# Kernel optimization log

Measured on AMD Instinct MI355X. Metric: run time of the kernel, lower is better.

## Reference

```python
import jax, jax.numpy as jnp
import numpy as np

OUT_F, IN_F = 16384, 4096
TOKENS = 8192
PALETTE = 256


def setup_inputs() -> dict:
    key = jax.random.key(0)
    k1, k2, k3, k4 = jax.random.split(key, 4)
    input = jax.random.normal(k1, (TOKENS, IN_F), dtype=jnp.float32)
    weight_idx = jax.random.randint(k2, (OUT_F, IN_F), 0, PALETTE, dtype=jnp.int32)
    lookup_table = jax.random.normal(k3, (PALETTE,), dtype=jnp.float32)
    bias = jax.random.normal(k4, (OUT_F,), dtype=jnp.float32)
    return {"input": input, "weight_idx": weight_idx, "lookup_table": lookup_table, "bias": bias}


def reference(input, weight_idx, lookup_table, bias):
    # Dequantize: LUT gather expands uint8 indices to full-precision weights [out, in]
    full_weights = lookup_table[weight_idx]
    # F.linear: y = x @ W^T + b
    return jnp.einsum('ti,oi->to', input, full_weights) + bias
```

## Files before the change

### kernel.cpp

```cpp
#include <hip/hip_runtime.h>
#include <stdint.h>

#define TOKENS 8192
#define OUT_F  16384
#define IN_F   4096

typedef short bf16x8 __attribute__((ext_vector_type(8)));
typedef float f32x4  __attribute__((ext_vector_type(4)));

__device__ __forceinline__ unsigned short bf16_rne(float f) {
    union { float f; unsigned int u; } v; v.f = f;
    unsigned int u = v.u;
    u += 0x7fffu + ((u >> 16) & 1u);
    return (unsigned short)(u >> 16);
}

__device__ __forceinline__ unsigned int pack_bf16x2(float a, float b) {
    return (unsigned int)bf16_rne(a) | ((unsigned int)bf16_rne(b) << 16);
}

__device__ __forceinline__ void async_cp16(const void* gptr, void* ldsptr) {
    __builtin_amdgcn_global_load_lds(
        (const __attribute__((address_space(1))) unsigned int*)gptr,
        (__attribute__((address_space(3))) unsigned int*)ldsptr,
        16, 0, 0);
}

__global__ __launch_bounds__(256) void cvt_input_kernel(
    const float* __restrict__ in, unsigned short* __restrict__ out, int n8)
{
    int i = blockIdx.x * 256 + threadIdx.x;
    if (i >= n8) return;
    size_t base = (size_t)i * 8;
    float4 a = *(const float4*)(in + base);
    float4 b = *(const float4*)(in + base + 4);
    uint4 p;
    p.x = pack_bf16x2(a.x, a.y);  p.y = pack_bf16x2(a.z, a.w);
    p.z = pack_bf16x2(b.x, b.y);  p.w = pack_bf16x2(b.z, b.w);
    *(uint4*)(out + base) = p;
}

__global__ __launch_bounds__(256) void dequant_kernel(
    const int* __restrict__ idx, const float* __restrict__ lut,
    unsigned short* __restrict__ out, int n8)
{
    __shared__ float slut[256];
    slut[threadIdx.x] = lut[threadIdx.x];
    __syncthreads();
    int i = blockIdx.x * 256 + threadIdx.x;
    if (i >= n8) return;
    size_t base = (size_t)i * 8;
    int4 i0 = *(const int4*)(idx + base);
    int4 i1 = *(const int4*)(idx + base + 4);
    uint4 p;
    p.x = pack_bf16x2(slut[i0.x], slut[i0.y]);
    p.y = pack_bf16x2(slut[i0.z], slut[i0.w]);
    p.z = pack_bf16x2(slut[i1.x], slut[i1.y]);
    p.w = pack_bf16x2(slut[i1.z], slut[i1.w]);
    *(uint4*)(out + base) = p;
}

__global__ __launch_bounds__(512, 2) void palett_gemm256(
    const unsigned short* __restrict__ A,
    const unsigned short* __restrict__ B,
    const float* __restrict__ bias,
    float* __restrict__ out)
{
    __shared__ __align__(16) char sm[131072];

    const int t    = threadIdx.x;
    const int w    = t >> 6;
    const int l    = t & 63;
    const int quad = l >> 4;
    const int r16  = l & 15;
    const int wr   = w >> 2;
    const int wc   = w & 3;

    const int orig = blockIdx.y * gridDim.x + blockIdx.x;
    const int swzb = (orig & 7) * 256 + (orig >> 3);
    const int n0   = (swzb & 63) << 8;
    const int m0   = (swzb >> 6) << 8;

    const int srow = w * 16 + (l >> 3);
    const int scol = ((l & 7) ^ (l >> 3)) << 3;
    const unsigned short* pA = A + (size_t)(m0 + srow) * IN_F + scol;
    const unsigned short* pB = B + (size_t)(n0 + srow) * IN_F + scol;

    const int cswz  = (r16 & 7) << 4;
    const int col0  = (quad * 16) ^ cswz;
    const int col1  = (64 + quad * 16) ^ cswz;
    const int arow  = r16 * 128;
    const int abase = wr * 16384;
    const int bbase = 32768 + (wc >> 1) * 16384 + (wc & 1) * 8192;

    f32x4  acc[8][4] = {};
    bf16x8 rA[4][2], rB0[2][2], rB1[2][2];

#define BARRIER() asm volatile("s_barrier" ::: "memory")

#define STAGE(P, HOFF, LOFF, KOFF) do {                                          \
    async_cp16((P) + (size_t)(HOFF) * IN_F + (KOFF), sm + (LOFF) + w * 2048);    \
    async_cp16((P) + (size_t)((HOFF) + 8) * IN_F + (KOFF),                       \
               sm + (LOFF) + w * 2048 + 1024);                                   \
} while (0)

#define READ_A(RB_, MH) do {                                                     \
    _Pragma("unroll")                                                            \
    for (int i_ = 0; i_ < 4; ++i_) {                                             \
        rA[i_][0] = *(const bf16x8*)(sm + (RB_) + abase + ((MH)*4 + i_)*2048 + arow + col0); \
        rA[i_][1] = *(const bf16x8*)(sm + (RB_) + abase + ((MH)*4 + i_)*2048 + arow + col1); \
    }                                                                            \
} while (0)

#define READ_B(DST, RB_, NH) do {                                                \
    _Pragma("unroll")                                                            \
    for (int j_ = 0; j_ < 2; ++j_) {                                             \
        DST[j_][0] = *(const bf16x8*)(sm + (RB_) + bbase + ((NH)*2 + j_)*2048 + arow + col0); \
        DST[j_][1] = *(const bf16x8*)(sm + (RB_) + bbase + ((NH)*2 + j_)*2048 + arow + col1); \
    }                                                                            \
} while (0)

#define MFMA_Q(MH, NH, RB) do {                                                  \
    _Pragma("unroll")                                                            \
    for (int i_ = 0; i_ < 4; ++i_) {                                             \
        _Pragma("unroll")                                                        \
        for (int j_ = 0; j_ < 2; ++j_) {                                         \
            acc[(MH)*4+i_][(NH)*2+j_] = __builtin_amdgcn_mfma_f32_16x16x32_bf16( \
                rA[i_][0], RB[j_][0], acc[(MH)*4+i_][(NH)*2+j_], 0, 0, 0);       \
            acc[(MH)*4+i_][(NH)*2+j_] = __builtin_amdgcn_mfma_f32_16x16x32_bf16( \
                rA[i_][1], RB[j_][1], acc[(MH)*4+i_][(NH)*2+j_], 0, 0, 0);       \
        }                                                                        \
    }                                                                            \
} while (0)

#define TILE(RB_, WB_, KB_, KA_) do {                                            \
                                        \
    STAGE(pB, 0,   (WB_) + 32768, KB_);                                          \
    STAGE(pB, 128, (WB_) + 49152, KB_);                                          \
    READ_A(RB_, 0);                                                              \
    READ_B(rB0, RB_, 0);                                                         \
    __builtin_amdgcn_s_setprio(1);                                               \
    MFMA_Q(0, 0, rB0);                                                           \
    __builtin_amdgcn_s_setprio(0);                                               \
    BARRIER();                                                                   \
        \
    READ_B(rB1, RB_, 1);                                                         \
    __builtin_amdgcn_s_setprio(1);                                               \
    MFMA_Q(0, 1, rB1);                                                           \
    __builtin_amdgcn_s_setprio(0);                                               \
    READ_A(RB_, 1);                                                              \
    asm volatile("s_waitcnt lgkmcnt(0)" ::: "memory");                           \
    BARRIER();           \
                                             \
    STAGE(pA, 0,   (RB_) + 0,     KA_);                                          \
    STAGE(pA, 128, (RB_) + 16384, KA_);                                          \
    __builtin_amdgcn_s_setprio(1);                                               \
    MFMA_Q(1, 0, rB0);                                                           \
    __builtin_amdgcn_s_setprio(0);                                               \
    BARRIER();                                                                   \
             \
    __builtin_amdgcn_s_setprio(1);                                               \
    MFMA_Q(1, 1, rB1);                                                           \
    __builtin_amdgcn_s_setprio(0);                                               \
    asm volatile("s_waitcnt vmcnt(4)" ::: "memory");                             \
    BARRIER();                                                                   \
} while (0)

    STAGE(pA, 0,   0,             0);
    STAGE(pA, 128, 16384,         0);
    STAGE(pB, 0,   32768,         0);
    STAGE(pB, 128, 49152,         0);
    STAGE(pA, 0,   65536 + 0,     64);
    STAGE(pA, 128, 65536 + 16384, 64);
    asm volatile("s_waitcnt vmcnt(4)" ::: "memory");
    BARRIER();

#pragma unroll 1
    for (int it = 0; it < 32; ++it) {
        const int tt = 2 * it;
        const int kB0 = ((tt + 1) & 63) * 64;
        const int kA0 = ((tt + 2) & 63) * 64;
        const int kB1 = ((tt + 2) & 63) * 64;
        const int kA1 = ((tt + 3) & 63) * 64;
        TILE(0,     65536, kB0, kA0);
        TILE(65536, 0,     kB1, kA1);
    }
    asm volatile("s_waitcnt vmcnt(0)" ::: "memory");

#undef TILE
#undef MFMA_Q
#undef READ_B
#undef READ_A
#undef STAGE
#undef BARRIER

    float bj[4];
#pragma unroll
    for (int j = 0; j < 4; ++j) bj[j] = bias[n0 + wc * 64 + j * 16 + r16];

#pragma unroll
    for (int mf = 0; mf < 8; ++mf) {
        const int mrow = m0 + wr * 128 + mf * 16 + quad * 4;
#pragma unroll
        for (int nf = 0; nf < 4; ++nf) {
            const int n = n0 + wc * 64 + nf * 16 + r16;
#pragma unroll
            for (int v = 0; v < 4; ++v)
                out[(size_t)(mrow + v) * OUT_F + n] = acc[mf][nf][v] + bj[nf];
        }
    }
}

__global__ __launch_bounds__(256) void palett_gemm_fused(
    const float* __restrict__ Af,
    const int* __restrict__ Widx,
    const float* __restrict__ lut,
    const float* __restrict__ bias,
    float* __restrict__ out)
{
    __shared__ __align__(16) unsigned short smA[128 * 32];
    __shared__ __align__(16) unsigned short smB[128 * 32];
    __shared__ float slut[256];

    const int t    = threadIdx.x;
    const int w    = t >> 6;
    const int l    = t & 63;
    const int quad = l >> 4;
    const int r16  = l & 15;
    const int wr   = w >> 1;
    const int wc   = w & 1;

    const int m0 = blockIdx.y * 128;
    const int n0 = blockIdx.x * 128;

    const int g0  = t * 8;
    const int row = g0 >> 5;
    const int col = g0 & 31;

    char* const smA_c = (char*)smA;
    char* const smB_c = (char*)smB;

    slut[t] = lut[t];
    __syncthreads();

    uint32_t aoff[4], boff[4];
#pragma unroll
    for (int i = 0; i < 4; ++i) {
        aoff[i] = (uint32_t)(((wr * 64 + i * 16 + r16) * 32 + quad * 8) * 2);
        boff[i] = (uint32_t)(((wc * 64 + i * 16 + r16) * 32 + quad * 8) * 2);
    }

    f32x4 acc[4][4] = {};

    const float* af0 = Af + (size_t)(m0 + row) * IN_F + col;
    const float* af1 = Af + (size_t)(m0 + row + 64) * IN_F + col;
    const int*   wi0 = Widx + (size_t)(n0 + row) * IN_F + col;
    const int*   wi1 = Widx + (size_t)(n0 + row + 64) * IN_F + col;

    for (int k0 = 0; k0 < IN_F; k0 += 32) {
        float4 x0 = *(const float4*)(af0 + k0);
        float4 x1 = *(const float4*)(af0 + k0 + 4);
        uint4 p;
        p.x = pack_bf16x2(x0.x, x0.y); p.y = pack_bf16x2(x0.z, x0.w);
        p.z = pack_bf16x2(x1.x, x1.y); p.w = pack_bf16x2(x1.z, x1.w);
        *(uint4*)(smA_c + t * 16) = p;
        x0 = *(const float4*)(af1 + k0);
        x1 = *(const float4*)(af1 + k0 + 4);
        p.x = pack_bf16x2(x0.x, x0.y); p.y = pack_bf16x2(x0.z, x0.w);
        p.z = pack_bf16x2(x1.x, x1.y); p.w = pack_bf16x2(x1.z, x1.w);
        *(uint4*)(smA_c + 4096 + t * 16) = p;

        int4 j0 = *(const int4*)(wi0 + k0);
        int4 j1 = *(const int4*)(wi0 + k0 + 4);
        p.x = pack_bf16x2(slut[j0.x], slut[j0.y]);
        p.y = pack_bf16x2(slut[j0.z], slut[j0.w]);
        p.z = pack_bf16x2(slut[j1.x], slut[j1.y]);
        p.w = pack_bf16x2(slut[j1.z], slut[j1.w]);
        *(uint4*)(smB_c + t * 16) = p;
        j0 = *(const int4*)(wi1 + k0);
        j1 = *(const int4*)(wi1 + k0 + 4);
        p.x = pack_bf16x2(slut[j0.x], slut[j0.y]);
        p.y = pack_bf16x2(slut[j0.z], slut[j0.w]);
        p.z = pack_bf16x2(slut[j1.x], slut[j1.y]);
        p.w = pack_bf16x2(slut[j1.z], slut[j1.w]);
        *(uint4*)(smB_c + 4096 + t * 16) = p;
        __syncthreads();

        bf16x8 afr[4], bfr[4];
#pragma unroll
        for (int i = 0; i < 4; ++i) afr[i] = *(const bf16x8*)(smA_c + aoff[i]);
#pragma unroll
        for (int j = 0; j < 4; ++j) bfr[j] = *(const bf16x8*)(smB_c + boff[j]);
#pragma unroll
        for (int i = 0; i < 4; ++i)
#pragma unroll
            for (int j = 0; j < 4; ++j)
                acc[i][j] = __builtin_amdgcn_mfma_f32_16x16x32_bf16(
                    afr[i], bfr[j], acc[i][j], 0, 0, 0);
        __syncthreads();
    }

    float bj[4];
#pragma unroll
    for (int j = 0; j < 4; ++j) bj[j] = bias[n0 + wc * 64 + j * 16 + r16];

#pragma unroll
    for (int i = 0; i < 4; ++i) {
        const int mbase = m0 + wr * 64 + i * 16 + quad * 4;
#pragma unroll
        for (int j = 0; j < 4; ++j) {
            const int n = n0 + wc * 64 + j * 16 + r16;
#pragma unroll
            for (int v = 0; v < 4; ++v) {
                out[(size_t)(mbase + v) * OUT_F + n] = acc[i][j][v] + bj[j];
            }
        }
    }
}

extern "C" void kernel_launch(void* const* d_in, const int* in_sizes, int n_in,
                              void* d_out, int out_size, void* d_ws, size_t ws_size,
                              hipStream_t stream) {
    const float* input = (const float*)d_in[0];
    const int*   widx  = (const int*)d_in[1];
    const float* lut   = (const float*)d_in[2];
    const float* bias  = (const float*)d_in[3];
    float* out = (float*)d_out;

    const size_t aBytes = (size_t)TOKENS * IN_F * sizeof(unsigned short);
    const size_t bBytes = (size_t)OUT_F  * IN_F * sizeof(unsigned short);

    if (ws_size >= aBytes + bBytes) {
        unsigned short* wsA = (unsigned short*)d_ws;
        unsigned short* wsB = (unsigned short*)((char*)d_ws + aBytes);
        const int nA8 = (TOKENS * IN_F) / 8;
        const int nB8 = (OUT_F  * IN_F) / 8;
        cvt_input_kernel<<<(nA8 + 255) / 256, 256, 0, stream>>>(input, wsA, nA8);
        dequant_kernel<<<(nB8 + 255) / 256, 256, 0, stream>>>(widx, lut, wsB, nB8);
        dim3 grid2(OUT_F / 256, TOKENS / 256);
        palett_gemm256<<<grid2, 512, 0, stream>>>(wsA, wsB, bias, out);
    } else {
        dim3 grid(OUT_F / 128, TOKENS / 128);
        palett_gemm_fused<<<grid, 256, 0, stream>>>(input, widx, lut, bias, out);
    }
}
```

Before: 1.580 ms.

## Switch GEMM main loop to 32x32x16 bf16 MFMA with k-step pipelined LDS reads

```diff
diff --git a/kernel.cpp b/kernel.cpp
--- a/kernel.cpp
+++ b/kernel.cpp
@@ -5,8 +5,9 @@
 #define OUT_F  16384
 #define IN_F   4096
 
-typedef short bf16x8 __attribute__((ext_vector_type(8)));
-typedef float f32x4  __attribute__((ext_vector_type(4)));
+typedef short bf16x8  __attribute__((ext_vector_type(8)));
+typedef float f32x4   __attribute__((ext_vector_type(4)));
+typedef float f32x16  __attribute__((ext_vector_type(16)));
 
 __device__ __forceinline__ unsigned short bf16_rne(float f) {
     union { float f; unsigned int u; } v; v.f = f;
@@ -71,8 +72,8 @@
     const int t    = threadIdx.x;
     const int w    = t >> 6;
     const int l    = t & 63;
-    const int quad = l >> 4;
-    const int r16  = l & 15;
+    const int l31  = l & 31;
+    const int hi   = l >> 5;
     const int wr   = w >> 2;
     const int wc   = w & 3;
 
@@ -86,17 +87,13 @@
     const unsigned short* pA = A + (size_t)(m0 + srow) * IN_F + scol;
     const unsigned short* pB = B + (size_t)(n0 + srow) * IN_F + scol;
 
-    const int cswz  = (r16 & 7) << 4;
-    const int col0  = (quad * 16) ^ cswz;
-    const int col1  = (64 + quad * 16) ^ cswz;
-    const int arow  = r16 * 128;
+    const int arow  = l31 * 128;
+    const int bcol  = ((hi ^ (l & 7)) << 4);
     const int abase = wr * 16384;
     const int bbase = 32768 + (wc >> 1) * 16384 + (wc & 1) * 8192;
 
-    f32x4  acc[8][4] = {};
-    bf16x8 rA[4][2], rB0[2][2], rB1[2][2];
-
-#define BARRIER() asm volatile("s_barrier" ::: "memory")
+    f32x16 acc[4][2] = {};
+    bf16x8 fA[2][4], fB[2][2];
 
 #define STAGE(P, HOFF, LOFF, KOFF) do {                                          \
     async_cp16((P) + (size_t)(HOFF) * IN_F + (KOFF), sm + (LOFF) + w * 2048);    \
@@ -104,66 +101,46 @@
                sm + (LOFF) + w * 2048 + 1024);                                   \
 } while (0)
 
-#define READ_A(RB_, MH) do {                                                     \
+#define READ_K(S_, RB_, KK_) do {                                                \
     _Pragma("unroll")                                                            \
-    for (int i_ = 0; i_ < 4; ++i_) {                                             \
-        rA[i_][0] = *(const bf16x8*)(sm + (RB_) + abase + ((MH)*4 + i_)*2048 + arow + col0); \
-        rA[i_][1] = *(const bf16x8*)(sm + (RB_) + abase + ((MH)*4 + i_)*2048 + arow + col1); \
+    for (int m_ = 0; m_ < 4; ++m_)                                               \
+        fA[S_][m_] = *(const bf16x8*)(sm + (RB_) + abase + m_ * 4096 + arow      \
+                                      + (((KK_) * 32) ^ bcol));                  \
+    _Pragma("unroll")                                                            \
+    for (int n_ = 0; n_ < 2; ++n_)                                               \
+        fB[S_][n_] = *(const bf16x8*)(sm + (RB_) + bbase + n_ * 4096 + arow      \
+                                      + (((KK_) * 32) ^ bcol));                  \
+} while (0)
+
+#define MFMA_K(S_) do {                                                          \
+    __builtin_amdgcn_s_setprio(1);                                               \
+    _Pragma("unroll")                                                            \
+    for (int m_ = 0; m_ < 4; ++m_) {                                             \
+        _Pragma("unroll")                                                        \
+        for (int n_ = 0; n_ < 2; ++n_)                                           \
+            acc[m_][n_] = __builtin_amdgcn_mfma_f32_32x32x16_bf16(               \
+                fA[S_][m_], fB[S_][n_], acc[m_][n_], 0, 0, 0);                   \
     }                                                                            \
+    __builtin_amdgcn_s_setprio(0);                                               \
 } while (0)
 
-#define READ_B(DST, RB_, NH) do {                                                \
-    _Pragma("unroll")                                                            \
-    for (int j_ = 0; j_ < 2; ++j_) {                                             \
-        DST[j_][0] = *(const bf16x8*)(sm + (RB_) + bbase + ((NH)*2 + j_)*2048 + arow + col0); \
-        DST[j_][1] = *(const bf16x8*)(sm + (RB_) + bbase + ((NH)*2 + j_)*2048 + arow + col1); \
-    }                                                                            \
-} while (0)
-
-#define MFMA_Q(MH, NH, RB) do {                                                  \
-    _Pragma("unroll")                                                            \
-    for (int i_ = 0; i_ < 4; ++i_) {                                             \
-        _Pragma("unroll")                                                        \
-        for (int j_ = 0; j_ < 2; ++j_) {                                         \
-            acc[(MH)*4+i_][(NH)*2+j_] = __builtin_amdgcn_mfma_f32_16x16x32_bf16( \
-                rA[i_][0], RB[j_][0], acc[(MH)*4+i_][(NH)*2+j_], 0, 0, 0);       \
-            acc[(MH)*4+i_][(NH)*2+j_] = __builtin_amdgcn_mfma_f32_16x16x32_bf16( \
-                rA[i_][1], RB[j_][1], acc[(MH)*4+i_][(NH)*2+j_], 0, 0, 0);       \
-        }                                                                        \
-    }                                                                            \
-} while (0)
-
 #define TILE(RB_, WB_, KB_, KA_) do {                                            \
-                                        \
+    READ_K(0, RB_, 0);                                                           \
     STAGE(pB, 0,   (WB_) + 32768, KB_);                                          \
+    READ_K(1, RB_, 1);                                                           \
+    MFMA_K(0);                                      \
     STAGE(pB, 128, (WB_) + 49152, KB_);                                          \
-    READ_A(RB_, 0);                                                              \
-    READ_B(rB0, RB_, 0);                                                         \
-    __builtin_amdgcn_s_setprio(1);                                               \
-    MFMA_Q(0, 0, rB0);                                                           \
-    __builtin_amdgcn_s_setprio(0);                                               \
-    BARRIER();                                                                   \
-        \
-    READ_B(rB1, RB_, 1);                                                         \
-    __builtin_amdgcn_s_setprio(1);                                               \
-    MFMA_Q(0, 1, rB1);                                                           \
-    __builtin_amdgcn_s_setprio(0);                                               \
-    READ_A(RB_, 1);                                                              \
-    asm volatile("s_waitcnt lgkmcnt(0)" ::: "memory");                           \
-    BARRIER();           \
-                                             \
+    READ_K(0, RB_, 2);                                                           \
+    MFMA_K(1);                                                         \
+    READ_K(1, RB_, 3);                                                           \
+    MFMA_K(0);                                                         \
+    asm volatile("s_waitcnt lgkmcnt(0)" ::: "memory");    \
+    asm volatile("s_barrier" ::: "memory");                \
     STAGE(pA, 0,   (RB_) + 0,     KA_);                                          \
     STAGE(pA, 128, (RB_) + 16384, KA_);                                          \
-    __builtin_amdgcn_s_setprio(1);                                               \
-    MFMA_Q(1, 0, rB0);                                                           \
-    __builtin_amdgcn_s_setprio(0);                                               \
-    BARRIER();                                                                   \
-             \
-    __builtin_amdgcn_s_setprio(1);                                               \
-    MFMA_Q(1, 1, rB1);                                                           \
-    __builtin_amdgcn_s_setprio(0);                                               \
-    asm volatile("s_waitcnt vmcnt(4)" ::: "memory");                             \
-    BARRIER();                                                                   \
+    MFMA_K(1);                                                         \
+    asm volatile("s_waitcnt vmcnt(4)" ::: "memory");       \
+    asm volatile("s_barrier" ::: "memory");                       \
 } while (0)
 
     STAGE(pA, 0,   0,             0);
@@ -173,11 +150,11 @@
     STAGE(pA, 0,   65536 + 0,     64);
     STAGE(pA, 128, 65536 + 16384, 64);
     asm volatile("s_waitcnt vmcnt(4)" ::: "memory");
-    BARRIER();
+    asm volatile("s_barrier" ::: "memory");
 
 #pragma unroll 1
     for (int it = 0; it < 32; ++it) {
-        const int tt = 2 * it;
+        const int tt  = 2 * it;
         const int kB0 = ((tt + 1) & 63) * 64;
         const int kA0 = ((tt + 2) & 63) * 64;
         const int kB1 = ((tt + 2) & 63) * 64;
@@ -188,25 +165,28 @@
     asm volatile("s_waitcnt vmcnt(0)" ::: "memory");
 
 #undef TILE
-#undef MFMA_Q
-#undef READ_B
-#undef READ_A
+#undef MFMA_K
+#undef READ_K
 #undef STAGE
-#undef BARRIER
-
-    float bj[4];
-#pragma unroll
-    for (int j = 0; j < 4; ++j) bj[j] = bias[n0 + wc * 64 + j * 16 + r16];
-
-#pragma unroll
-    for (int mf = 0; mf < 8; ++mf) {
-        const int mrow = m0 + wr * 128 + mf * 16 + quad * 4;
-#pragma unroll
-        for (int nf = 0; nf < 4; ++nf) {
-            const int n = n0 + wc * 64 + nf * 16 + r16;
-#pragma unroll
-            for (int v = 0; v < 4; ++v)
-                out[(size_t)(mrow + v) * OUT_F + n] = acc[mf][nf][v] + bj[nf];
+
+    float bj[2];
+#pragma unroll
+    for (int nj = 0; nj < 2; ++nj) bj[nj] = bias[n0 + wc * 64 + nj * 32 + l31];
+
+#pragma unroll
+    for (int mi = 0; mi < 4; ++mi) {
+        const int mrow = m0 + wr * 128 + mi * 32 + hi * 4;
+#pragma unroll
+        for (int nj = 0; nj < 2; ++nj) {
+            const int n = n0 + wc * 64 + nj * 32 + l31;
+#pragma unroll
+            for (int g = 0; g < 4; ++g) {
+#pragma unroll
+                for (int v = 0; v < 4; ++v) {
+                    out[(size_t)(mrow + g * 8 + v) * OUT_F + n] =
+                        acc[mi][nj][g * 4 + v] + bj[nj];
+                }
+            }
         }
     }
 }
```

After: 1.680 ms. +6.3%, slower.
